# Performance work log

Hardware: AMD Instinct MI355X
Metric: run time of the kernel (lower is better)

Reference implementation:

```python
import jax, jax.numpy as jnp
import numpy as np

N_NODES = 50000
N_EDGES = 1600000
IN_FEAT, H_FEAT, OUT_FEAT, N_CLASSES = 256, 128, 64, 8


def setup_inputs() -> dict:
    key = jax.random.key(0)
    ks = jax.random.split(key, 8)
    seq = jax.random.normal(ks[0], (N_NODES, IN_FEAT), dtype=jnp.float32)
    edge_index = jax.random.randint(ks[1], (2, N_EDGES), 0, N_NODES, dtype=jnp.int64)
    # GCNConv weights (stored as [in, out]) and biases; Glorot-ish scale
    W1 = jax.random.normal(ks[2], (IN_FEAT, H_FEAT), dtype=jnp.float32) / np.sqrt(IN_FEAT)
    b1 = jnp.zeros((H_FEAT,), dtype=jnp.float32)
    W2 = jax.random.normal(ks[3], (H_FEAT, OUT_FEAT), dtype=jnp.float32) / np.sqrt(H_FEAT)
    b2 = jnp.zeros((OUT_FEAT,), dtype=jnp.float32)
    Wc = jax.random.normal(ks[4], (OUT_FEAT, N_CLASSES), dtype=jnp.float32) / np.sqrt(OUT_FEAT)
    bc = jnp.zeros((N_CLASSES,), dtype=jnp.float32)
    return {"seq": seq, "edge_index": edge_index,
            "W1": W1, "b1": b1, "W2": W2, "b2": b2, "Wc": Wc, "bc": bc}


def _gcn_conv(x, W, b, src, dst, norm, n_nodes):
    # PyG GCNConv: h = x @ W, then symmetric-normalized aggregation to dst, + bias
    h = x @ W                                   # [N, out]
    msg = h[src] * norm[:, None]                # [E+N, out] gather + scale
    out = jax.ops.segment_sum(msg, dst, num_segments=n_nodes)  # scatter-add
    return out + b


def reference(seq, edge_index, W1, b1, W2, b2, Wc, bc):
    n = seq.shape[0]
    loops = jnp.arange(n, dtype=edge_index.dtype)
    src = jnp.concatenate([edge_index[0], loops])  # add self-loops
    dst = jnp.concatenate([edge_index[1], loops])
    # symmetric normalization deg^{-1/2}[src] * deg^{-1/2}[dst]
    deg = jax.ops.segment_sum(jnp.ones_like(dst, dtype=seq.dtype), dst, num_segments=n)
    dinv = jnp.where(deg > 0, jax.lax.rsqrt(deg), 0.0)
    norm = dinv[src] * dinv[dst]                  # [E+N]
    res1 = _gcn_conv(seq, W1, b1, src, dst, norm, n)
    res2 = _gcn_conv(res1, W2, b2, src, dst, norm, n)
    return res2 @ Wc + bc
```

## Files before the change

### kernel.cpp

```cpp
#include <hip/hip_runtime.h>
#include <hip/hip_bf16.h>
#include <stdint.h>

#define NN 50000
#define NE 1600000
#define BSH 7
#define NBK 391
#define CAP 4608
#define NSB 256
#define ECH 6250
#define EPAIR 3125

__global__ __launch_bounds__(1024) void k_iw(const float* __restrict__ W1, const float* __restrict__ b1,
                                             const float* __restrict__ W2, const float* __restrict__ b2,
                                             const float* __restrict__ Wc, const float* __restrict__ bc,
                                             float* __restrict__ Wcombo, float* __restrict__ c12,
                                             const int* __restrict__ dst, int* __restrict__ bh){
  const int t = threadIdx.x;
  if (blockIdx.x == 0){
    __shared__ float M1[1024];
    {
      int k = t >> 3, c = t & 7;
      float s = 0.f;
      for (int j = 0; j < 64; ++j) s += W2[k * 64 + j] * Wc[j * 8 + c];
      M1[t] = s;
    }
    __syncthreads();
    for (int idx = t; idx < 2048; idx += 1024){
      int i = idx >> 3, c = idx & 7;
      float s = 0.f;
      for (int k = 0; k < 128; ++k) s += W1[i * 128 + k] * M1[k * 8 + c];
      Wcombo[idx] = s;
    }
    if (t < 8){
      float s = 0.f;
      for (int k = 0; k < 128; ++k) s += b1[k] * M1[k * 8 + t];
      c12[t] = s;
    } else if (t < 16){
      int c = t - 8;
      float s = bc[c];
      for (int k = 0; k < 64; ++k) s += b2[k] * Wc[k * 8 + c];
      c12[t] = s;
    }
  } else {
    __shared__ int h[4 * NBK];
    const int hb = blockIdx.x - 1;
    for (int i = t; i < 4 * NBK; i += 1024) h[i] = 0;
    __syncthreads();
    const int g = (t >> 8) * NBK;
    const int2* dp = (const int2*)(dst + hb * ECH);
    for (int i = t; i < EPAIR; i += 1024){
      int2 d = dp[i];
      atomicAdd(&h[g + (d.x >> BSH)], 1);
      atomicAdd(&h[g + (d.y >> BSH)], 1);
    }
    __syncthreads();
    for (int i = t; i < NBK; i += 1024)
      bh[(size_t)hb * NBK + i] = h[i] + h[NBK + i] + h[2 * NBK + i] + h[3 * NBK + i];
  }
}

__global__ __launch_bounds__(1024) void k_by(const int* __restrict__ bh, int* __restrict__ boff,
                                             int* __restrict__ btot,
                                             const float* __restrict__ X, const float* __restrict__ Wcombo,
                                             float* __restrict__ Yraw){
  const int t = threadIdx.x;
  if (blockIdx.x < 98){
    __shared__ int lds[1024];
    const int tt = t & 255;
    const int b = blockIdx.x * 4 + (t >> 8);
    const bool ok = b < NBK;
    int v = ok ? bh[(size_t)tt * NBK + b] : 0;
    lds[t] = v;
    __syncthreads();
    for (int ofs = 1; ofs < 256; ofs <<= 1){
      int tmp = (tt >= ofs) ? lds[t - ofs] : 0;
      __syncthreads();
      lds[t] += tmp;
      __syncthreads();
    }
    if (ok) boff[(size_t)tt * NBK + b] = lds[t] - v;
    if (ok && tt == 255) btot[b] = lds[t];
  } else {
    __shared__ float Wl[2048];
    for (int i = t; i < 2048; i += 1024) Wl[i] = Wcombo[i];
    __syncthreads();
    int gid = (blockIdx.x - 98) * 1024 + t;
    int row = gid >> 3, c = gid & 7;
    if (row >= NN) return;
    const float* Xr = X + (size_t)row * 256;
    float acc = 0.f;
    #pragma unroll 8
    for (int k = 0; k < 256; k += 4){
      float4 x = *(const float4*)(Xr + k);
      acc += x.x * Wl[k * 8 + c] + x.y * Wl[(k + 1) * 8 + c]
           + x.z * Wl[(k + 2) * 8 + c] + x.w * Wl[(k + 3) * 8 + c];
    }
    Yraw[(size_t)row * 8 + c] = acc;
  }
}

__global__ __launch_bounds__(1024) void k_scat(const int* __restrict__ src, const int* __restrict__ dst,
                                               const int* __restrict__ boff, uint32_t* __restrict__ ebuf){
  __shared__ int ctr[NBK];
  const int t = threadIdx.x;
  for (int i = t; i < NBK; i += 1024)
    ctr[i] = i * CAP + boff[(size_t)blockIdx.x * NBK + i];
  __syncthreads();
  const int2* dp = (const int2*)(dst + blockIdx.x * ECH);
  const int2* sp = (const int2*)(src + blockIdx.x * ECH);
  for (int i = t; i < EPAIR; i += 1024){
    int2 d = dp[i];
    int2 s = sp[i];
    int p0 = atomicAdd(&ctr[d.x >> BSH], 1);
    ebuf[p0] = ((uint32_t)s.x << 16) | (uint32_t)d.x;
    int p1 = atomicAdd(&ctr[d.y >> BSH], 1);
    ebuf[p1] = ((uint32_t)s.y << 16) | (uint32_t)d.y;
  }
}

__global__ __launch_bounds__(512) void k_csr(const uint32_t* __restrict__ ebuf, const int* __restrict__ btot,
                                             float* __restrict__ dinv, int2* __restrict__ offs2,
                                             unsigned short* __restrict__ csr){
  __shared__ uint32_t lede[CAP];
  __shared__ unsigned short lcsr[CAP];
  __shared__ int h[128];
  __shared__ int sb[128];
  const int t = threadIdx.x;
  const int b = blockIdx.x;
  const int base = b * CAP;
  const int cnt = btot[b];
  for (int i = t; i < cnt; i += 512) lede[i] = ebuf[base + i];
  if (t < 128) h[t] = 0;
  __syncthreads();
  for (int i = t; i < cnt; i += 512)
    atomicAdd(&h[lede[i] & 127], 1);
  __syncthreads();
  int deg = (t < 128) ? h[t] : 0;
  for (int ofs = 1; ofs < 128; ofs <<= 1){
    int tv = (t >= ofs && t < 128) ? h[t - ofs] : 0;
    __syncthreads();
    if (t < 128) h[t] += tv;
    __syncthreads();
  }
  int excl = (t < 128) ? (h[t] - deg) : 0;
  int node = (b << BSH) + t;
  if (t < 128 && node < NN){
    dinv[node] = rsqrtf((float)(deg + 1));
    offs2[node] = make_int2(base + excl, base + excl + deg);
  }
  __syncthreads();
  if (t < 128) sb[t] = excl;
  __syncthreads();
  for (int i = t; i < cnt; i += 512){
    uint32_t v = lede[i];
    int p = atomicAdd(&sb[v & 127], 1);
    lcsr[p] = (unsigned short)(v >> 16);
  }
  __syncthreads();
  uint32_t* dstw = (uint32_t*)(csr + base);
  const uint32_t* srcw = (const uint32_t*)lcsr;
  int nw = (cnt + 1) >> 1;
  for (int i = t; i < nw; i += 512) dstw[i] = srcw[i];
}

__global__ __launch_bounds__(256) void k_agg1(const unsigned short* __restrict__ csr, const int2* __restrict__ offs2,
                                              const float* __restrict__ dinv, const float* __restrict__ Y,
                                              float* __restrict__ U, float* __restrict__ V){
  int gid = blockIdx.x * 256 + threadIdx.x;
  int node = gid >> 3, c = gid & 7;
  if (node >= NN) return;
  int2 oe = offs2[node];
  int e = oe.x;
  const int e1 = oe.y;
  float a = 0.f, vd = 0.f;
  for (; e + 4 <= e1; e += 4){
    int s0 = csr[e], s1 = csr[e + 1], s2 = csr[e + 2], s3 = csr[e + 3];
    float d0 = dinv[s0], d1 = dinv[s1], d2 = dinv[s2], d3 = dinv[s3];
    float y0 = Y[(size_t)s0 * 8 + c], y1 = Y[(size_t)s1 * 8 + c];
    float y2 = Y[(size_t)s2 * 8 + c], y3 = Y[(size_t)s3 * 8 + c];
    a += (d0 * y0 + d1 * y1) + (d2 * y2 + d3 * y3);
    vd += (d0 + d1) + (d2 + d3);
  }
  for (; e < e1; ++e){
    int s0 = csr[e];
    float d0 = dinv[s0];
    a += d0 * Y[(size_t)s0 * 8 + c];
    vd += d0;
  }
  float di = dinv[node];
  U[(size_t)node * 8 + c] = di * di * (a + di * Y[(size_t)node * 8 + c]);
  if (c == 0) V[node] = di * (vd + di);
}

__global__ __launch_bounds__(256) void k_agg2(const unsigned short* __restrict__ csr, const int2* __restrict__ offs2,
                                              const float* __restrict__ dinv, const float* __restrict__ U,
                                              const float* __restrict__ V, const float* __restrict__ c12,
                                              float* __restrict__ O){
  int gid = blockIdx.x * 256 + threadIdx.x;
  int node = gid >> 3, c = gid & 7;
  if (node >= NN) return;
  int2 oe = offs2[node];
  int e = oe.x;
  const int e1 = oe.y;
  float a = 0.f;
  for (; e + 4 <= e1; e += 4){
    int s0 = csr[e], s1 = csr[e + 1], s2 = csr[e + 2], s3 = csr[e + 3];
    float y0 = U[(size_t)s0 * 8 + c], y1 = U[(size_t)s1 * 8 + c];
    float y2 = U[(size_t)s2 * 8 + c], y3 = U[(size_t)s3 * 8 + c];
    a += (y0 + y1) + (y2 + y3);
  }
  for (; e < e1; ++e){
    int s0 = csr[e];
    a += U[(size_t)s0 * 8 + c];
  }
  float di = dinv[node];
  O[(size_t)node * 8 + c] = di * (a + U[(size_t)node * 8 + c]) + V[node] * c12[c] + c12[8 + c];
}

extern "C" void kernel_launch(void* const* d_in, const int* in_sizes, int n_in,
                              void* d_out, int out_size, void* d_ws, size_t ws_size,
                              hipStream_t stream) {
  const float* seq = (const float*)d_in[0];
  const int*   ei  = (const int*)d_in[1];
  const int*   esrc = ei;
  const int*   edst = ei + NE;
  const float* W1 = (const float*)d_in[2];
  const float* b1 = (const float*)d_in[3];
  const float* W2 = (const float*)d_in[4];
  const float* b2 = (const float*)d_in[5];
  const float* Wc = (const float*)d_in[6];
  const float* bc = (const float*)d_in[7];
  float* out = (float*)d_out;

  char* ws = (char*)d_ws;
  size_t o = 0;
  auto alloc = [&](size_t bytes) -> void* {
    void* p = ws + o;
    o += (bytes + 255) & ~(size_t)255;
    return p;
  };
  int*      bh    = (int*)alloc((size_t)NSB * NBK * 4);
  int*      boff  = (int*)alloc((size_t)NSB * NBK * 4);
  int*      btot  = (int*)alloc((size_t)NBK * 4);
  uint32_t* ebuf  = (uint32_t*)alloc((size_t)NBK * CAP * 4);
  unsigned short* csr = (unsigned short*)alloc((size_t)NBK * CAP * 2);
  int2*     offs2 = (int2*)alloc((size_t)NN * 8);
  float*    dinv  = (float*)alloc((size_t)NN * 4);
  float*    Wcb   = (float*)alloc(2048 * 4);
  float*    c12   = (float*)alloc(16 * 4);
  float*    Yraw  = (float*)alloc((size_t)NN * 8 * 4);
  float*    U     = (float*)alloc((size_t)NN * 8 * 4);
  float*    V     = (float*)alloc((size_t)NN * 4);

  k_iw     <<<1 + NSB, 1024, 0, stream>>>(W1, b1, W2, b2, Wc, bc, Wcb, c12, edst, bh);
  k_by     <<<98 + 391, 1024, 0, stream>>>(bh, boff, btot, seq, Wcb, Yraw);
  k_scat   <<<NSB, 1024, 0, stream>>>(esrc, edst, boff, ebuf);
  k_csr    <<<NBK, 512, 0, stream>>>(ebuf, btot, dinv, offs2, csr);
  k_agg1   <<<1563, 256, 0, stream>>>(csr, offs2, dinv, Yraw, U, V);
  k_agg2   <<<1563, 256, 0, stream>>>(csr, offs2, dinv, U, V, c12, out);
}
```

Measured before the change: 93.81 us.

## Move dense X·W projection from scan kernel into edge-scatter kernel

The bucket prefix scan becomes its own kernel of 391 blocks with 256 threads. The dense seq×Wcombo projection blocks now share a launch with the edge scatter-to-buckets blocks instead of with the scan. This overlaps the bandwidth-heavy X read with the atomic-heavy scatter and leaves the scan as a small, quick kernel. Kernel count stays the same; the cost is a heavier mixed kernel whose two block types may compete for the same CUs.

```diff
diff --git a/kernel.cpp b/kernel.cpp
--- a/kernel.cpp
+++ b/kernel.cpp
@@ -60,32 +60,48 @@
   }
 }
 
-__global__ __launch_bounds__(1024) void k_by(const int* __restrict__ bh, int* __restrict__ boff,
-                                             int* __restrict__ btot,
+__global__ __launch_bounds__(NSB) void k_bscan(const int* __restrict__ bh, int* __restrict__ boff,
+                                               int* __restrict__ btot){
+  __shared__ int lds[NSB];
+  const int b = blockIdx.x;
+  int v = bh[(size_t)threadIdx.x * NBK + b];
+  lds[threadIdx.x] = v;
+  __syncthreads();
+  for (int ofs = 1; ofs < NSB; ofs <<= 1){
+    int t = (threadIdx.x >= ofs) ? lds[threadIdx.x - ofs] : 0;
+    __syncthreads();
+    lds[threadIdx.x] += t;
+    __syncthreads();
+  }
+  boff[(size_t)threadIdx.x * NBK + b] = lds[threadIdx.x] - v;
+  if (threadIdx.x == NSB - 1) btot[b] = lds[NSB - 1];
+}
+
+__global__ __launch_bounds__(1024) void k_sy(const int* __restrict__ src, const int* __restrict__ dst,
+                                             const int* __restrict__ boff, uint32_t* __restrict__ ebuf,
                                              const float* __restrict__ X, const float* __restrict__ Wcombo,
                                              float* __restrict__ Yraw){
   const int t = threadIdx.x;
-  if (blockIdx.x < 98){
-    __shared__ int lds[1024];
-    const int tt = t & 255;
-    const int b = blockIdx.x * 4 + (t >> 8);
-    const bool ok = b < NBK;
-    int v = ok ? bh[(size_t)tt * NBK + b] : 0;
-    lds[t] = v;
-    __syncthreads();
-    for (int ofs = 1; ofs < 256; ofs <<= 1){
-      int tmp = (tt >= ofs) ? lds[t - ofs] : 0;
-      __syncthreads();
-      lds[t] += tmp;
-      __syncthreads();
-    }
-    if (ok) boff[(size_t)tt * NBK + b] = lds[t] - v;
-    if (ok && tt == 255) btot[b] = lds[t];
+  if (blockIdx.x < NSB){
+    __shared__ int ctr[NBK];
+    for (int i = t; i < NBK; i += 1024)
+      ctr[i] = i * CAP + boff[(size_t)blockIdx.x * NBK + i];
+    __syncthreads();
+    const int2* dp = (const int2*)(dst + blockIdx.x * ECH);
+    const int2* sp = (const int2*)(src + blockIdx.x * ECH);
+    for (int i = t; i < EPAIR; i += 1024){
+      int2 d = dp[i];
+      int2 s = sp[i];
+      int p0 = atomicAdd(&ctr[d.x >> BSH], 1);
+      ebuf[p0] = ((uint32_t)s.x << 16) | (uint32_t)d.x;
+      int p1 = atomicAdd(&ctr[d.y >> BSH], 1);
+      ebuf[p1] = ((uint32_t)s.y << 16) | (uint32_t)d.y;
+    }
   } else {
     __shared__ float Wl[2048];
     for (int i = t; i < 2048; i += 1024) Wl[i] = Wcombo[i];
     __syncthreads();
-    int gid = (blockIdx.x - 98) * 1024 + t;
+    int gid = (blockIdx.x - NSB) * 1024 + t;
     int row = gid >> 3, c = gid & 7;
     if (row >= NN) return;
     const float* Xr = X + (size_t)row * 256;
@@ -97,25 +113,6 @@
            + x.z * Wl[(k + 2) * 8 + c] + x.w * Wl[(k + 3) * 8 + c];
     }
     Yraw[(size_t)row * 8 + c] = acc;
-  }
-}
-
-__global__ __launch_bounds__(1024) void k_scat(const int* __restrict__ src, const int* __restrict__ dst,
-                                               const int* __restrict__ boff, uint32_t* __restrict__ ebuf){
-  __shared__ int ctr[NBK];
-  const int t = threadIdx.x;
-  for (int i = t; i < NBK; i += 1024)
-    ctr[i] = i * CAP + boff[(size_t)blockIdx.x * NBK + i];
-  __syncthreads();
-  const int2* dp = (const int2*)(dst + blockIdx.x * ECH);
-  const int2* sp = (const int2*)(src + blockIdx.x * ECH);
-  for (int i = t; i < EPAIR; i += 1024){
-    int2 d = dp[i];
-    int2 s = sp[i];
-    int p0 = atomicAdd(&ctr[d.x >> BSH], 1);
-    ebuf[p0] = ((uint32_t)s.x << 16) | (uint32_t)d.x;
-    int p1 = atomicAdd(&ctr[d.y >> BSH], 1);
-    ebuf[p1] = ((uint32_t)s.y << 16) | (uint32_t)d.y;
   }
 }
 
@@ -253,10 +250,10 @@
   float*    U     = (float*)alloc((size_t)NN * 8 * 4);
   float*    V     = (float*)alloc((size_t)NN * 4);
 
-  k_iw     <<<1 + NSB, 1024, 0, stream>>>(W1, b1, W2, b2, Wc, bc, Wcb, c12, edst, bh);
-  k_by     <<<98 + 391, 1024, 0, stream>>>(bh, boff, btot, seq, Wcb, Yraw);
-  k_scat   <<<NSB, 1024, 0, stream>>>(esrc, edst, boff, ebuf);
-  k_csr    <<<NBK, 512, 0, stream>>>(ebuf, btot, dinv, offs2, csr);
-  k_agg1   <<<1563, 256, 0, stream>>>(csr, offs2, dinv, Yraw, U, V);
-  k_agg2   <<<1563, 256, 0, stream>>>(csr, offs2, dinv, U, V, c12, out);
-}
+  k_iw    <<<1 + NSB, 1024, 0, stream>>>(W1, b1, W2, b2, Wc, bc, Wcb, c12, edst, bh);
+  k_bscan <<<NBK, NSB, 0, stream>>>(bh, boff, btot);
+  k_sy    <<<NSB + 391, 1024, 0, stream>>>(esrc, edst, boff, ebuf, seq, Wcb, Yraw);
+  k_csr   <<<NBK, 512, 0, stream>>>(ebuf, btot, dinv, offs2, csr);
+  k_agg1  <<<1563, 256, 0, stream>>>(csr, offs2, dinv, Yraw, U, V);
+  k_agg2  <<<1563, 256, 0, stream>>>(csr, offs2, dinv, U, V, c12, out);
+}
```

Measured after the change: 91.43 us. 1.03x faster.
